# Optimization experiments

Measured on AMD Instinct MI355X. Metric: run time of the kernel, lower is better.

## Reference

```python
import jax, jax.numpy as jnp
import numpy as np

B, IN, OUT, K, TOPK = 1024, 4096, 4096, 64, 64


def setup_inputs() -> dict:
    key = jax.random.key(0)
    k0, k1, k2, k3 = jax.random.split(key, 4)
    return {
        "x": jax.random.normal(k0, (B, K), dtype=jnp.float32),
        "weight": jax.random.normal(k1, (OUT, IN), dtype=jnp.float32) / np.float32(np.sqrt(IN)),
        "bias": jax.random.normal(k2, (OUT,), dtype=jnp.float32) * 0.01,
        "prev_idx": jax.random.randint(k3, (B, K), 0, IN),
        "top_k": TOPK,
    }


def reference(x, weight, bias, prev_idx, top_k):
    # Per-sample column gather of the weight matrix: (OUT, B, K)
    gathered = jnp.take(weight, prev_idx, axis=1)
    # Batched matvec (torch.bmm with input.unsqueeze(-1)) + bias -> (B, OUT)
    result = jnp.einsum('obk,bk->bo', gathered, x) + bias
    # top-k select; torch.gather(result, 1, topk_indices) == top-k values
    vals, sel = jax.lax.top_k(result, top_k)
    return vals, sel
```

## Files before the change

kernel.cpp:

```cpp
#include <hip/hip_runtime.h>
#include <stdint.h>
#include <math.h>


#define NB    1024
#define NIN   4096
#define NOUT  4096
#define NK    64
#define NTOPK 64

__device__ __forceinline__ int SWZ(int i) { return i ^ ((i >> 3) & 7); }

__global__ __launch_bounds__(256) void pack_kernel(const float* __restrict__ x,
                                                   const int* __restrict__ idx,
                                                   int2* __restrict__ fused) {
    int tid = blockIdx.x * 256 + threadIdx.x;
    int k = tid >> 10;
    int b = tid & 1023;
    int   iv = idx[(b << 6) + k];
    float xv = x[(b << 6) + k];
    fused[tid] = make_int2(SWZ(iv) << 4, __float_as_int(xv));
}

__global__ __launch_bounds__(512) void gemm_kernel(const int2* __restrict__ fused,
                                                   const float* __restrict__ W,
                                                   const float* __restrict__ bias,
                                                   double* __restrict__ C) {
    __shared__ float4 Wt[NIN];
    const int t  = threadIdx.x;
    const int o0 = blockIdx.x * 4;

    const float4* w0p = reinterpret_cast<const float4*>(W + (size_t)(o0 + 0) * NIN);
    const float4* w1p = reinterpret_cast<const float4*>(W + (size_t)(o0 + 1) * NIN);
    const float4* w2p = reinterpret_cast<const float4*>(W + (size_t)(o0 + 2) * NIN);
    const float4* w3p = reinterpret_cast<const float4*>(W + (size_t)(o0 + 3) * NIN);
#pragma unroll
    for (int m = 0; m < 2; ++m) {
        int j = t + m * 512;
        float4 r0 = w0p[j], r1 = w1p[j], r2 = w2p[j], r3 = w3p[j];
        int i0 = j << 2;
        Wt[SWZ(i0 + 0)] = make_float4(r0.x, r1.x, r2.x, r3.x);
        Wt[SWZ(i0 + 1)] = make_float4(r0.y, r1.y, r2.y, r3.y);
        Wt[SWZ(i0 + 2)] = make_float4(r0.z, r1.z, r2.z, r3.z);
        Wt[SWZ(i0 + 3)] = make_float4(r0.w, r1.w, r2.w, r3.w);
    }
    __syncthreads();

    double acc[2][4];
    for (int r = 0; r < 4; ++r) {
        double bd = (double)bias[o0 + r];
        acc[0][r] = bd;
        acc[1][r] = bd;
    }

    const int b0 = t << 1;
    const int4* fp = reinterpret_cast<const int4*>(fused + b0);

#pragma unroll 4
    for (int k = 0; k < NK; ++k) {
        int4 f = fp[k * 512];
        const float4 w0 = *reinterpret_cast<const float4*>(
            reinterpret_cast<const char*>(Wt) + f.x);
        const float4 w1 = *reinterpret_cast<const float4*>(
            reinterpret_cast<const char*>(Wt) + f.z);
        double x0 = (double)__int_as_float(f.y);
        double x1 = (double)__int_as_float(f.w);
        acc[0][0] += x0 * (double)w0.x; acc[0][1] += x0 * (double)w0.y;
        acc[0][2] += x0 * (double)w0.z; acc[0][3] += x0 * (double)w0.w;
        acc[1][0] += x1 * (double)w1.x; acc[1][1] += x1 * (double)w1.y;
        acc[1][2] += x1 * (double)w1.z; acc[1][3] += x1 * (double)w1.w;
    }

    for (int c = 0; c < 2; ++c) {
        double* dst = C + (size_t)(b0 + c) * NOUT + o0;
        dst[0] = acc[c][0]; dst[1] = acc[c][1];
        dst[2] = acc[c][2]; dst[3] = acc[c][3];
    }
}

__device__ __forceinline__ unsigned keyf(double d) {
    unsigned u = __float_as_uint((float)d);
    return (u & 0x80000000u) ? ~u : (u | 0x80000000u);
}

__global__ __launch_bounds__(256) void topk_kernel(const double* __restrict__ C,
                                                   float* __restrict__ outv,
                                                   float* __restrict__ outi) {
    __shared__ unsigned hist[4096];
    __shared__ double   cval[1024];
    __shared__ int      cidx[1024];
    __shared__ unsigned part[256];
    __shared__ int      sBstar;
    __shared__ unsigned sCnt;

    const int t = threadIdx.x;
    const double* row = C + (size_t)blockIdx.x * NOUT;

    double v[16];
#pragma unroll
    for (int q = 0; q < 16; ++q) v[q] = row[q * 256 + t];

    for (int j = t; j < 4096; j += 256) hist[j] = 0u;
    if (t == 0) sCnt = 0u;
    __syncthreads();

#pragma unroll
    for (int q = 0; q < 16; ++q)
        atomicAdd(&hist[keyf(v[q]) >> 20], 1u);
    __syncthreads();

    {
        unsigned s = 0;
        for (int q = 0; q < 16; ++q) s += hist[t * 16 + q];
        part[t] = s;
    }
    __syncthreads();

    if (t < 64) {
        unsigned c0 = part[4 * t + 0], c1 = part[4 * t + 1];
        unsigned c2 = part[4 * t + 2], c3 = part[4 * t + 3];
        unsigned s = c0 + c1 + c2 + c3;
        unsigned suf = s;
        for (int off = 1; off < 64; off <<= 1) {
            unsigned xx = __shfl_down(suf, off);
            if (t + off < 64) suf += xx;
        }
        unsigned below = suf - s;
        part[4 * t + 3] = below + c3;
        part[4 * t + 2] = below + c3 + c2;
        part[4 * t + 1] = below + c3 + c2 + c1;
        part[4 * t + 0] = below + s;
    }
    __syncthreads();

    {
        unsigned run = (t < 255) ? part[t + 1] : 0u;
        for (int q = 15; q >= 0; --q) {
            int bin = t * 16 + q;
            unsigned cge = run + hist[bin];
            if (cge >= 64u && run < 64u) sBstar = bin;
            run = cge;
        }
    }
    __syncthreads();

    const unsigned Bstar = (unsigned)sBstar;
#pragma unroll
    for (int q = 0; q < 16; ++q) {
        if ((keyf(v[q]) >> 20) >= Bstar) {
            unsigned pos = atomicAdd(&sCnt, 1u);
            if (pos < 1024u) { cval[pos] = v[q]; cidx[pos] = q * 256 + t; }
        }
    }
    __syncthreads();

    int M = (int)sCnt; if (M > 1024) M = 1024;
    int n = 64; while (n < M) n <<= 1;
    for (int j = M + t; j < n; j += 256) { cval[j] = -INFINITY; cidx[j] = 0x7fffffff; }
    __syncthreads();

    for (int kk = 2; kk <= n; kk <<= 1) {
        for (int jj = kk >> 1; jj > 0; jj >>= 1) {
            for (int i = t; i < n; i += 256) {
                int l = i ^ jj;
                if (l > i) {
                    double v1 = cval[i], v2 = cval[l];
                    int    i1 = cidx[i], i2 = cidx[l];
                    bool first = (v1 > v2) || (v1 == v2 && i1 < i2);
                    bool asc   = ((i & kk) == 0);
                    if (first != asc) {
                        cval[i] = v2; cval[l] = v1;
                        cidx[i] = i2; cidx[l] = i1;
                    }
                }
            }
            __syncthreads();
        }
    }

    if (t < 64) {
        outv[(blockIdx.x << 6) + t] = (float)cval[t];
        outi[(blockIdx.x << 6) + t] = (float)cidx[t];
    }
}

extern "C" void kernel_launch(void* const* d_in, const int* in_sizes, int n_in,
                              void* d_out, int out_size, void* d_ws, size_t ws_size,
                              hipStream_t stream) {
    const float* x    = (const float*)d_in[0];
    const float* W    = (const float*)d_in[1];
    const float* bias = (const float*)d_in[2];
    const int*   idx  = (const int*)d_in[3];

    char*   ws    = (char*)d_ws;
    double* C     = (double*)ws;
    int2*   fused = (int2*)(ws + (size_t)NB * NOUT * sizeof(double));

    float* outv = (float*)d_out;
    float* outi = outv + NB * NTOPK;

    pack_kernel<<<(NB * NK) / 256, 256, 0, stream>>>(x, idx, fused);
    gemm_kernel<<<NOUT / 4, 512, 0, stream>>>(fused, W, bias, C);
    topk_kernel<<<NB, 256, 0, stream>>>(C, outv, outi);
}
```

Measured before the change: 154.2 us.

## Use one batch row per thread in gemm and vectorize C accesses

The gemm kernel now launches 1024 threads per block, one per batch row. Each thread accumulates both k-pairs into a single row and writes its four outputs as two double2 stores. The pack kernel emits int4 records holding two k entries per batch row. The top-k kernel reads C with double2 loads and remaps candidate indices to match, and it transposes the histogram layout in shared memory to reduce bank conflicts in the per-thread bin scans. The goal is fewer memory transactions and less LDS conflict, at the cost of a longer serial k loop per thread and heavier register pressure under the new launch bounds.

After: 158.1 us. 2.5% more time.

```diff
diff --git a/kernel.cpp b/kernel.cpp
--- a/kernel.cpp
+++ b/kernel.cpp
@@ -13,32 +13,32 @@
 
 __global__ __launch_bounds__(256) void pack_kernel(const float* __restrict__ x,
                                                    const int* __restrict__ idx,
-                                                   int2* __restrict__ fused) {
+                                                   int4* __restrict__ fused) {
     int tid = blockIdx.x * 256 + threadIdx.x;
-    int k = tid >> 10;
-    int b = tid & 1023;
-    int   iv = idx[(b << 6) + k];
-    float xv = x[(b << 6) + k];
-    fused[tid] = make_int2(SWZ(iv) << 4, __float_as_int(xv));
-}
-
-__global__ __launch_bounds__(512) void gemm_kernel(const int2* __restrict__ fused,
-                                                   const float* __restrict__ W,
-                                                   const float* __restrict__ bias,
-                                                   double* __restrict__ C) {
+    int k2 = tid >> 10;
+    int b  = tid & 1023;
+    int base = (b << 6) + (k2 << 1);
+    int   i0 = idx[base],  i1 = idx[base + 1];
+    float x0 = x[base],    x1 = x[base + 1];
+    fused[tid] = make_int4(SWZ(i0) << 4, __float_as_int(x0),
+                           SWZ(i1) << 4, __float_as_int(x1));
+}
+
+__global__ __launch_bounds__(1024, 8) void gemm_kernel(const int4* __restrict__ fused,
+                                                       const float* __restrict__ W,
+                                                       const float* __restrict__ bias,
+                                                       double* __restrict__ C) {
     __shared__ float4 Wt[NIN];
     const int t  = threadIdx.x;
     const int o0 = blockIdx.x * 4;
 
-    const float4* w0p = reinterpret_cast<const float4*>(W + (size_t)(o0 + 0) * NIN);
-    const float4* w1p = reinterpret_cast<const float4*>(W + (size_t)(o0 + 1) * NIN);
-    const float4* w2p = reinterpret_cast<const float4*>(W + (size_t)(o0 + 2) * NIN);
-    const float4* w3p = reinterpret_cast<const float4*>(W + (size_t)(o0 + 3) * NIN);
-#pragma unroll
-    for (int m = 0; m < 2; ++m) {
-        int j = t + m * 512;
-        float4 r0 = w0p[j], r1 = w1p[j], r2 = w2p[j], r3 = w3p[j];
-        int i0 = j << 2;
+    {
+        const float4* w0p = reinterpret_cast<const float4*>(W + (size_t)(o0 + 0) * NIN);
+        const float4* w1p = reinterpret_cast<const float4*>(W + (size_t)(o0 + 1) * NIN);
+        const float4* w2p = reinterpret_cast<const float4*>(W + (size_t)(o0 + 2) * NIN);
+        const float4* w3p = reinterpret_cast<const float4*>(W + (size_t)(o0 + 3) * NIN);
+        float4 r0 = w0p[t], r1 = w1p[t], r2 = w2p[t], r3 = w3p[t];
+        int i0 = t << 2;
         Wt[SWZ(i0 + 0)] = make_float4(r0.x, r1.x, r2.x, r3.x);
         Wt[SWZ(i0 + 1)] = make_float4(r0.y, r1.y, r2.y, r3.y);
         Wt[SWZ(i0 + 2)] = make_float4(r0.z, r1.z, r2.z, r3.z);
@@ -46,42 +46,37 @@
     }
     __syncthreads();
 
-    double acc[2][4];
-    for (int r = 0; r < 4; ++r) {
-        double bd = (double)bias[o0 + r];
-        acc[0][r] = bd;
-        acc[1][r] = bd;
-    }
-
-    const int b0 = t << 1;
-    const int4* fp = reinterpret_cast<const int4*>(fused + b0);
+    double acc[4];
+#pragma unroll
+    for (int r = 0; r < 4; ++r) acc[r] = (double)bias[o0 + r];
+
+    const int4* fp = fused + t;
 
 #pragma unroll 4
-    for (int k = 0; k < NK; ++k) {
-        int4 f = fp[k * 512];
+    for (int k2 = 0; k2 < NK / 2; ++k2) {
+        int4 f = fp[k2 << 10];
         const float4 w0 = *reinterpret_cast<const float4*>(
             reinterpret_cast<const char*>(Wt) + f.x);
         const float4 w1 = *reinterpret_cast<const float4*>(
             reinterpret_cast<const char*>(Wt) + f.z);
         double x0 = (double)__int_as_float(f.y);
+        acc[0] += x0 * (double)w0.x; acc[1] += x0 * (double)w0.y;
+        acc[2] += x0 * (double)w0.z; acc[3] += x0 * (double)w0.w;
         double x1 = (double)__int_as_float(f.w);
-        acc[0][0] += x0 * (double)w0.x; acc[0][1] += x0 * (double)w0.y;
-        acc[0][2] += x0 * (double)w0.z; acc[0][3] += x0 * (double)w0.w;
-        acc[1][0] += x1 * (double)w1.x; acc[1][1] += x1 * (double)w1.y;
-        acc[1][2] += x1 * (double)w1.z; acc[1][3] += x1 * (double)w1.w;
-    }
-
-    for (int c = 0; c < 2; ++c) {
-        double* dst = C + (size_t)(b0 + c) * NOUT + o0;
-        dst[0] = acc[c][0]; dst[1] = acc[c][1];
-        dst[2] = acc[c][2]; dst[3] = acc[c][3];
-    }
+        acc[0] += x1 * (double)w1.x; acc[1] += x1 * (double)w1.y;
+        acc[2] += x1 * (double)w1.z; acc[3] += x1 * (double)w1.w;
+    }
+
+    double2* dst = reinterpret_cast<double2*>(C + (size_t)t * NOUT + o0);
+    dst[0] = make_double2(acc[0], acc[1]);
+    dst[1] = make_double2(acc[2], acc[3]);
 }
 
 __device__ __forceinline__ unsigned keyf(double d) {
     unsigned u = __float_as_uint((float)d);
     return (u & 0x80000000u) ? ~u : (u | 0x80000000u);
 }
+__device__ __forceinline__ int HADDR(int bin) { return ((bin & 15) << 8) | (bin >> 4); }
 
 __global__ __launch_bounds__(256) void topk_kernel(const double* __restrict__ C,
                                                    float* __restrict__ outv,
@@ -94,11 +89,14 @@
     __shared__ unsigned sCnt;
 
     const int t = threadIdx.x;
-    const double* row = C + (size_t)blockIdx.x * NOUT;
+    const double2* row2 = reinterpret_cast<const double2*>(C + (size_t)blockIdx.x * NOUT);
 
     double v[16];
 #pragma unroll
-    for (int q = 0; q < 16; ++q) v[q] = row[q * 256 + t];
+    for (int q = 0; q < 8; ++q) {
+        double2 d = row2[q * 256 + t];
+        v[2 * q] = d.x; v[2 * q + 1] = d.y;
+    }
 
     for (int j = t; j < 4096; j += 256) hist[j] = 0u;
     if (t == 0) sCnt = 0u;
@@ -106,12 +104,13 @@
 
 #pragma unroll
     for (int q = 0; q < 16; ++q)
-        atomicAdd(&hist[keyf(v[q]) >> 20], 1u);
+        atomicAdd(&hist[HADDR(keyf(v[q]) >> 20)], 1u);
     __syncthreads();
 
     {
         unsigned s = 0;
-        for (int q = 0; q < 16; ++q) s += hist[t * 16 + q];
+#pragma unroll
+        for (int q = 0; q < 16; ++q) s += hist[(q << 8) | t];
         part[t] = s;
     }
     __syncthreads();
@@ -135,10 +134,10 @@
 
     {
         unsigned run = (t < 255) ? part[t + 1] : 0u;
+#pragma unroll
         for (int q = 15; q >= 0; --q) {
-            int bin = t * 16 + q;
-            unsigned cge = run + hist[bin];
-            if (cge >= 64u && run < 64u) sBstar = bin;
+            unsigned cge = run + hist[(q << 8) | t];
+            if (cge >= 64u && run < 64u) sBstar = t * 16 + q;
             run = cge;
         }
     }
@@ -149,7 +148,10 @@
     for (int q = 0; q < 16; ++q) {
         if ((keyf(v[q]) >> 20) >= Bstar) {
             unsigned pos = atomicAdd(&sCnt, 1u);
-            if (pos < 1024u) { cval[pos] = v[q]; cidx[pos] = q * 256 + t; }
+            if (pos < 1024u) {
+                cval[pos] = v[q];
+                cidx[pos] = (q >> 1) * 512 + 2 * t + (q & 1);
+            }
         }
     }
     __syncthreads();
@@ -194,12 +196,12 @@
 
     char*   ws    = (char*)d_ws;
     double* C     = (double*)ws;
-    int2*   fused = (int2*)(ws + (size_t)NB * NOUT * sizeof(double));
+    int4*   fused = (int4*)(ws + (size_t)NB * NOUT * sizeof(double));
 
     float* outv = (float*)d_out;
     float* outi = outv + NB * NTOPK;
 
-    pack_kernel<<<(NB * NK) / 256, 256, 0, stream>>>(x, idx, fused);
-    gemm_kernel<<<NOUT / 4, 512, 0, stream>>>(fused, W, bias, C);
+    pack_kernel<<<(NB * NK / 2) / 256, 256, 0, stream>>>(x, idx, fused);
+    gemm_kernel<<<NOUT / 4, 1024, 0, stream>>>(fused, W, bias, C);
     topk_kernel<<<NB, 256, 0, stream>>>(C, outv, outi);
 }
```
